# Kernel tuning notes

Hardware: AMD Instinct MI355X
Metric: run time of the kernel (lower is better)

Reference implementation:

```python
import jax, jax.numpy as jnp
import numpy as np

H = 128          # hidden_dim
L = 3            # num_layers
EPS = 1e-5       # BatchNorm eps


def setup_inputs() -> dict:
    key = jax.random.key(0)
    ks = jax.random.split(key, 12)
    B, N = 32, 8192
    s = 0.05
    x = jax.random.normal(ks[0], (B, N, 2), dtype=jnp.float32)
    mask = jnp.ones((B, N), dtype=jnp.float32)
    # parameters, stored as [in, out]
    emb_w = jax.random.normal(ks[1], (2, H), jnp.float32) * s
    emb_b = jnp.zeros((H,), jnp.float32)
    lin_w = jax.random.normal(ks[2], (L, H, H), jnp.float32) * s
    lin_b = jnp.zeros((L, H), jnp.float32)
    nb_w = jax.random.normal(ks[3], (L, H, H), jnp.float32) * s
    nb_b = jnp.zeros((L, H), jnp.float32)
    bn_g = jnp.ones((L, H), jnp.float32)
    bn_b = jnp.zeros((L, H), jnp.float32)
    out1_w = jax.random.normal(ks[4], (H, H // 2), jnp.float32) * s
    out1_b = jnp.zeros((H // 2,), jnp.float32)
    out2_w = jax.random.normal(ks[5], (H // 2, 2), jnp.float32) * s
    out2_b = jnp.zeros((2,), jnp.float32)
    return dict(x=x, mask=mask, emb_w=emb_w, emb_b=emb_b,
                lin_w=lin_w, lin_b=lin_b, nb_w=nb_w, nb_b=nb_b,
                bn_g=bn_g, bn_b=bn_b, out1_w=out1_w, out1_b=out1_b,
                out2_w=out2_w, out2_b=out2_b)


def reference(x, mask, emb_w, emb_b, lin_w, lin_b, nb_w, nb_b,
              bn_g, bn_b, out1_w, out1_b, out2_w, out2_b):
    m = mask[..., None]                     # [B, N, 1]
    h = x @ emb_w + emb_b                   # [B, N, H]
    for i in range(L):
        # graph conv: self transform + ring-neighbor (roll) transform
        nsum = jnp.roll(h, 1, axis=1) + jnp.roll(h, -1, axis=1)
        h_new = (h @ lin_w[i] + lin_b[i] + nsum @ nb_w[i] + nb_b[i]) * m
        # BatchNorm1d (training-mode batch stats over batch*nodes per channel)
        mean = jnp.mean(h_new, axis=(0, 1))
        var = jnp.mean(jnp.square(h_new - mean), axis=(0, 1))  # biased var
        h_new = (h_new - mean) * jax.lax.rsqrt(var + EPS) * bn_g[i] + bn_b[i]
        h_new = jax.nn.relu(h_new)          # dropout treated as identity (eval)
        h = h + h_new                       # residual
    out = jax.nn.relu(h @ out1_w + out1_b) @ out2_w + out2_b  # [B, N, 2]
    return out * m
```

## Files before the change

### kernel.cpp

```cpp
#include <hip/hip_runtime.h>
#include <cstddef>

#define H      128
#define NBATCH 32
#define NN     8192
#define RTOT   (NBATCH*NN)
#define NLAYER 3
#define BNEPS  1e-5f
#define NSLOT  16
#define CNPB   128
#define NTILEC (RTOT/CNPB)
#define HNPB   64
#define HS_STRIDE 136

typedef _Float16 f16;
typedef __attribute__((ext_vector_type(8))) _Float16 half8;
typedef __attribute__((ext_vector_type(4))) float f32x4;

__device__ __forceinline__ void unpackh8(uint4 pk, float* d) {
    const f16* hp = (const f16*)&pk;
    #pragma unroll
    for (int i = 0; i < 8; ++i) d[i] = (float)hp[i];
}
__device__ __forceinline__ uint4 packh8(const float* s) {
    uint4 pk;
    f16* hp = (f16*)&pk;
    #pragma unroll
    for (int i = 0; i < 8; ++i) hp[i] = (f16)s[i];
    return pk;
}

__device__ __forceinline__ void load_bfrags(
    const f16* __restrict__ Wt, half8 bW[2][4], int colbase, int l15, int quad)
{
    #pragma unroll
    for (int nt = 0; nt < 2; ++nt) {
        int nrow = colbase + nt * 16 + l15;
        #pragma unroll
        for (int ks = 0; ks < 4; ++ks)
            bW[nt][ks] = *((const half8*)(Wt + nrow * 128 + ks * 32 + quad * 8));
    }
}

__device__ __forceinline__ void conv_mfma8(
    const f16* __restrict__ hs, const half8 bWl[2][4], const half8 bWn[2][4],
    f32x4 acc[8][2], int l15, int quad)
{
    #pragma unroll
    for (int mt = 0; mt < 8; ++mt) {
        acc[mt][0] = (f32x4){0.f, 0.f, 0.f, 0.f};
        acc[mt][1] = (f32x4){0.f, 0.f, 0.f, 0.f};
    }
    #pragma unroll
    for (int ks = 0; ks < 4; ++ks) {
        #pragma unroll
        for (int mt = 0; mt < 8; ++mt) {
            int row = mt * 16 + l15;
            const f16* base = hs + row * HS_STRIDE + ks * 32 + quad * 8;
            half8 hm = *((const half8*)(base + HS_STRIDE));
            half8 hd = *((const half8*)(base));
            half8 hu = *((const half8*)(base + 2 * HS_STRIDE));
            half8 an = hd + hu;
            acc[mt][0] = __builtin_amdgcn_mfma_f32_16x16x32_f16(hm, bWl[0][ks], acc[mt][0], 0, 0, 0);
            acc[mt][1] = __builtin_amdgcn_mfma_f32_16x16x32_f16(hm, bWl[1][ks], acc[mt][1], 0, 0, 0);
            acc[mt][0] = __builtin_amdgcn_mfma_f32_16x16x32_f16(an, bWn[0][ks], acc[mt][0], 0, 0, 0);
            acc[mt][1] = __builtin_amdgcn_mfma_f32_16x16x32_f16(an, bWn[1][ks], acc[mt][1], 0, 0, 0);
        }
    }
}

__global__ __launch_bounds__(256) void k_prep(
    const float* __restrict__ lin_w, const float* __restrict__ nb_w,
    f16* __restrict__ Wlt, f16* __restrict__ Wnt)
{
    int id = blockIdx.x * 256 + threadIdx.x;
    int mat = id / 49152;
    int r   = id - mat * 49152;
    int l   = r >> 14;
    int r2  = r & 16383;
    int k   = r2 >> 7;
    int n   = r2 & 127;
    const float* src = mat ? nb_w : lin_w;
    f16*         dst = mat ? Wnt  : Wlt;
    dst[l * 16384 + n * 128 + k] = (f16)src[l * 16384 + k * 128 + n];
}

__device__ __forceinline__ void conv_epilogue_c(
    f32x4 acc[8][2], const float bsum[2], const float* __restrict__ msk,
    f16* __restrict__ hnb, float* __restrict__ gstats,
    int tile, int wave, int quad, int lane, int slot)
{
    uint2* out2 = (uint2*)hnb;
    float s[2] = {0.f, 0.f}, ss[2] = {0.f, 0.f};
    #pragma unroll
    for (int nt = 0; nt < 2; ++nt) {
        #pragma unroll
        for (int mt = 0; mt < 8; ++mt) {
            f16 v4[4];
            #pragma unroll
            for (int reg = 0; reg < 4; ++reg) {
                int lrow = mt * 16 + quad * 4 + reg;
                float v = (acc[mt][nt][reg] + bsum[nt]) * msk[lrow];
                v4[reg] = (f16)v;
                s[nt] += v; ss[nt] += v * v;
            }
            size_t chunk = ((size_t)tile * 4 + wave) * 16 + mt * 2 + nt;
            out2[chunk * 64 + lane] = *((const uint2*)v4);
        }
    }
    #pragma unroll
    for (int nt = 0; nt < 2; ++nt) {
        s[nt]  += __shfl_xor(s[nt], 16);  s[nt]  += __shfl_xor(s[nt], 32);
        ss[nt] += __shfl_xor(ss[nt], 16); ss[nt] += __shfl_xor(ss[nt], 32);
    }
    if (lane < 16) {
        int colbase = wave * 32;
        #pragma unroll
        for (int nt = 0; nt < 2; ++nt) {
            int col = colbase + nt * 16 + lane;
            atomicAdd(&gstats[slot * 2 * H + col],     s[nt]);
            atomicAdd(&gstats[slot * 2 * H + H + col], ss[nt]);
        }
    }
}

__device__ __forceinline__ void conv_epilogue_rm(
    f32x4 acc[8][2], const float bsum[2], const float* __restrict__ msk,
    f16* __restrict__ tr, f16* __restrict__ hnb, float* __restrict__ gstats,
    int r0, int colbase, int l15, int quad, int lane, int t, int slot)
{
    float s[2] = {0.f, 0.f}, ss[2] = {0.f, 0.f};
    #pragma unroll
    for (int nt = 0; nt < 2; ++nt) {
        int col = colbase + nt * 16 + l15;
        #pragma unroll
        for (int mt = 0; mt < 8; ++mt)
            #pragma unroll
            for (int reg = 0; reg < 4; ++reg) {
                int lrow = mt * 16 + quad * 4 + reg;
                float v = (acc[mt][nt][reg] + bsum[nt]) * msk[lrow];
                tr[lrow * HS_STRIDE + col] = (f16)v;
                s[nt] += v; ss[nt] += v * v;
            }
    }
    #pragma unroll
    for (int nt = 0; nt < 2; ++nt) {
        s[nt]  += __shfl_xor(s[nt], 16);  s[nt]  += __shfl_xor(s[nt], 32);
        ss[nt] += __shfl_xor(ss[nt], 16); ss[nt] += __shfl_xor(ss[nt], 32);
    }
    if (lane < 16)
        #pragma unroll
        for (int nt = 0; nt < 2; ++nt) {
            int col = colbase + nt * 16 + lane;
            atomicAdd(&gstats[slot * 2 * H + col],     s[nt]);
            atomicAdd(&gstats[slot * 2 * H + H + col], ss[nt]);
        }
    __syncthreads();
    for (int i = t; i < CNPB * 16; i += 256) {
        int row = i >> 4, g = i & 15;
        *((uint4*)(hnb + (size_t)(r0 + row) * H + g * 8)) =
            *((const uint4*)(tr + row * HS_STRIDE + g * 8));
    }
}

__global__ __launch_bounds__(256) void k_conv0f(
    const float* __restrict__ x, const float* __restrict__ ew,
    const float* __restrict__ eb,
    const f16* __restrict__ Wlt, const f16* __restrict__ Wnt,
    const float* __restrict__ bl, const float* __restrict__ bnb,
    const float* __restrict__ mask,
    f16* __restrict__ hnb, float* __restrict__ gstats)
{
    __shared__ __align__(16) f16 hs[(CNPB + 2) * HS_STRIDE];
    __shared__ float ews[3 * H], msk[CNPB];
    const int t = threadIdx.x, lane = t & 63;
    const int l15 = lane & 15, quad = lane >> 4;
    const int wave = t >> 6;
    const int colbase = wave * 32;
    const int r0 = blockIdx.x * CNPB;
    const int batch = r0 >> 13, n0 = r0 & (NN - 1);

    half8 bWl[2][4], bWn[2][4];
    load_bfrags(Wlt, bWl, colbase, l15, quad);
    load_bfrags(Wnt, bWn, colbase, l15, quad);
    float bsum[2];
    #pragma unroll
    for (int nt = 0; nt < 2; ++nt) {
        int col = colbase + nt * 16 + l15;
        bsum[nt] = bl[col] + bnb[col];
    }
    for (int c = t; c < H; c += 256) {
        ews[c] = ew[c]; ews[H + c] = ew[H + c]; ews[2 * H + c] = eb[c];
    }
    if (t < CNPB) msk[t] = mask[r0 + t];
    __syncthreads();

    for (int i = t; i < (CNPB + 2) * 16; i += 256) {
        int row = i >> 4, g = i & 15;
        int n = (n0 + row - 1 + NN) & (NN - 1);
        const float* xp = x + 2 * ((size_t)batch * NN + n);
        float x0 = xp[0], x1 = xp[1];
        f16 o[8];
        #pragma unroll
        for (int e = 0; e < 8; ++e) {
            int c = g * 8 + e;
            o[e] = (f16)fmaf(x1, ews[H + c], fmaf(x0, ews[c], ews[2 * H + c]));
        }
        *((uint4*)(hs + row * HS_STRIDE + g * 8)) = *((const uint4*)o);
    }
    __syncthreads();

    f32x4 acc[8][2];
    conv_mfma8(hs, bWl, bWn, acc, l15, quad);
    conv_epilogue_c(acc, bsum, msk, hnb, gstats,
                    blockIdx.x, wave, quad, lane, blockIdx.x & (NSLOT - 1));
}

__global__ __launch_bounds__(256) void k_conv0f_rm(
    const float* __restrict__ x, const float* __restrict__ ew,
    const float* __restrict__ eb,
    const f16* __restrict__ Wlt, const f16* __restrict__ Wnt,
    const float* __restrict__ bl, const float* __restrict__ bnb,
    const float* __restrict__ mask,
    f16* __restrict__ hnb, float* __restrict__ gstats)
{
    __shared__ __align__(16) f16 hs[(CNPB + 2) * HS_STRIDE];
    __shared__ float ews[3 * H], msk[CNPB];
    const int t = threadIdx.x, lane = t & 63;
    const int l15 = lane & 15, quad = lane >> 4;
    const int wave = t >> 6;
    const int colbase = wave * 32;
    const int r0 = blockIdx.x * CNPB;
    const int batch = r0 >> 13, n0 = r0 & (NN - 1);

    half8 bWl[2][4], bWn[2][4];
    load_bfrags(Wlt, bWl, colbase, l15, quad);
    load_bfrags(Wnt, bWn, colbase, l15, quad);
    float bsum[2];
    #pragma unroll
    for (int nt = 0; nt < 2; ++nt) {
        int col = colbase + nt * 16 + l15;
        bsum[nt] = bl[col] + bnb[col];
    }
    for (int c = t; c < H; c += 256) {
        ews[c] = ew[c]; ews[H + c] = ew[H + c]; ews[2 * H + c] = eb[c];
    }
    if (t < CNPB) msk[t] = mask[r0 + t];
    __syncthreads();

    for (int i = t; i < (CNPB + 2) * 16; i += 256) {
        int row = i >> 4, g = i & 15;
        int n = (n0 + row - 1 + NN) & (NN - 1);
        const float* xp = x + 2 * ((size_t)batch * NN + n);
        float x0 = xp[0], x1 = xp[1];
        f16 o[8];
        #pragma unroll
        for (int e = 0; e < 8; ++e) {
            int c = g * 8 + e;
            o[e] = (f16)fmaf(x1, ews[H + c], fmaf(x0, ews[c], ews[2 * H + c]));
        }
        *((uint4*)(hs + row * HS_STRIDE + g * 8)) = *((const uint4*)o);
    }
    __syncthreads();

    f32x4 acc[8][2];
    conv_mfma8(hs, bWl, bWn, acc, l15, quad);
    __syncthreads();
    conv_epilogue_rm(acc, bsum, msk, hs, hnb, gstats,
                     r0, colbase, l15, quad, lane, t, blockIdx.x & (NSLOT - 1));
}

__global__ __launch_bounds__(256) void k_conv(
    const f16* __restrict__ hb,
    const f16* __restrict__ Wlt, const f16* __restrict__ Wnt,
    const float* __restrict__ bl, const float* __restrict__ bnb,
    const float* __restrict__ mask,
    f16* __restrict__ hnb, float* __restrict__ gstats)
{
    __shared__ __align__(16) f16 hs[(CNPB + 2) * HS_STRIDE];
    __shared__ float msk[CNPB];
    const int t = threadIdx.x, lane = t & 63;
    const int l15 = lane & 15, quad = lane >> 4;
    const int wave = t >> 6;
    const int colbase = wave * 32;
    const int r0 = blockIdx.x * CNPB;
    const int batch = r0 >> 13, n0 = r0 & (NN - 1);

    half8 bWl[2][4], bWn[2][4];
    load_bfrags(Wlt, bWl, colbase, l15, quad);
    load_bfrags(Wnt, bWn, colbase, l15, quad);
    float bsum[2];
    #pragma unroll
    for (int nt = 0; nt < 2; ++nt) {
        int col = colbase + nt * 16 + l15;
        bsum[nt] = bl[col] + bnb[col];
    }
    if (t < CNPB) msk[t] = mask[r0 + t];

    for (int i = t; i < (CNPB + 2) * 16; i += 256) {
        int row = i >> 4, g = i & 15;
        int n = (n0 + row - 1 + NN) & (NN - 1);
        *((uint4*)(hs + row * HS_STRIDE + g * 8)) =
            *((const uint4*)(hb + ((size_t)(batch * NN + n)) * H + g * 8));
    }
    __syncthreads();

    f32x4 acc[8][2];
    conv_mfma8(hs, bWl, bWn, acc, l15, quad);
    conv_epilogue_c(acc, bsum, msk, hnb, gstats,
                    blockIdx.x, wave, quad, lane, blockIdx.x & (NSLOT - 1));
}

__global__ __launch_bounds__(256) void k_cn1(
    const float* __restrict__ x, const float* __restrict__ ew,
    const float* __restrict__ eb, const f16* __restrict__ hnA,
    const float* __restrict__ scl0,
    const f16* __restrict__ Wlt, const f16* __restrict__ Wnt,
    const float* __restrict__ bl, const float* __restrict__ bnb,
    const float* __restrict__ mask,
    f16* __restrict__ HB, f16* __restrict__ hnB, float* __restrict__ gst1)
{
    __shared__ __align__(16) f16 hs[(CNPB + 2) * HS_STRIDE];
    __shared__ float ews[3 * H], sclA[2 * H], msk[CNPB];
    const int t = threadIdx.x, lane = t & 63;
    const int l15 = lane & 15, quad = lane >> 4;
    const int wave = t >> 6;
    const int colbase = wave * 32;
    const int r0 = blockIdx.x * CNPB;
    const int batch = r0 >> 13, n0 = r0 & (NN - 1);

    half8 bWl[2][4], bWn[2][4];
    load_bfrags(Wlt, bWl, colbase, l15, quad);
    load_bfrags(Wnt, bWn, colbase, l15, quad);
    float bsum[2];
    #pragma unroll
    for (int nt = 0; nt < 2; ++nt) {
        int col = colbase + nt * 16 + l15;
        bsum[nt] = bl[col] + bnb[col];
    }
    for (int c = t; c < H; c += 256) {
        ews[c] = ew[c]; ews[H + c] = ew[H + c]; ews[2 * H + c] = eb[c];
        sclA[c] = scl0[c]; sclA[H + c] = scl0[H + c];
    }
    if (t < CNPB) msk[t] = mask[r0 + t];
    __syncthreads();

    for (int i = t; i < (CNPB + 2) * 16; i += 256) {
        int row = i >> 4, g = i & 15;
        int n = (n0 + row - 1 + NN) & (NN - 1);
        size_t base = (size_t)batch * NN + n;
        const float* xp = x + 2 * base;
        float x0 = xp[0], x1 = xp[1];
        uint4 pa = *((const uint4*)(hnA + base * H + g * 8));
        float va[8];
        unpackh8(pa, va);
        f16 o[8];
        #pragma unroll
        for (int e = 0; e < 8; ++e) {
            int c = g * 8 + e;
            float h0 = fmaf(x1, ews[H + c], fmaf(x0, ews[c], ews[2 * H + c]));
            o[e] = (f16)(h0 + fmaxf(fmaf(va[e], sclA[c], sclA[H + c]), 0.f));
        }
        *((uint4*)(hs + row * HS_STRIDE + g * 8)) = *((const uint4*)o);
    }
    __syncthreads();

    f32x4 acc[8][2];
    conv_mfma8(hs, bWl, bWn, acc, l15, quad);

    for (int i = t; i < CNPB * 16; i += 256) {
        int row = i >> 4, g = i & 15;
        *((uint4*)(HB + (size_t)(r0 + row) * H + g * 8)) =
            *((const uint4*)(hs + (row + 1) * HS_STRIDE + g * 8));
    }
    __syncthreads();

    conv_epilogue_rm(acc, bsum, msk, hs, hnB, gst1,
                     r0, colbase, l15, quad, lane, t, blockIdx.x & (NSLOT - 1));
}

__global__ __launch_bounds__(256) void k_cn2(
    const f16* __restrict__ HB, const f16* __restrict__ hnB,
    const float* __restrict__ scl1,
    const f16* __restrict__ Wlt, const f16* __restrict__ Wnt,
    const float* __restrict__ bl, const float* __restrict__ bnb,
    const float* __restrict__ mask,
    f16* __restrict__ hnA, float* __restrict__ gst2)
{
    __shared__ __align__(16) f16 hs[(CNPB + 2) * HS_STRIDE];
    __shared__ float sclA[2 * H], msk[CNPB];
    const int t = threadIdx.x, lane = t & 63;
    const int l15 = lane & 15, quad = lane >> 4;
    const int wave = t >> 6;
    const int colbase = wave * 32;
    const int r0 = blockIdx.x * CNPB;
    const int batch = r0 >> 13, n0 = r0 & (NN - 1);

    half8 bWl[2][4], bWn[2][4];
    load_bfrags(Wlt, bWl, colbase, l15, quad);
    load_bfrags(Wnt, bWn, colbase, l15, quad);
    float bsum[2];
    #pragma unroll
    for (int nt = 0; nt < 2; ++nt) {
        int col = colbase + nt * 16 + l15;
        bsum[nt] = bl[col] + bnb[col];
    }
    for (int c = t; c < H; c += 256) {
        sclA[c] = scl1[c]; sclA[H + c] = scl1[H + c];
    }
    if (t < CNPB) msk[t] = mask[r0 + t];
    __syncthreads();

    for (int i = t; i < (CNPB + 2) * 16; i += 256) {
        int row = i >> 4, g = i & 15;
        int n = (n0 + row - 1 + NN) & (NN - 1);
        size_t off = ((size_t)batch * NN + n) * H + g * 8;
        uint4 ph = *((const uint4*)(HB + off));
        uint4 pn = *((const uint4*)(hnB + off));
        float vh[8], vn[8];
        unpackh8(ph, vh);
        unpackh8(pn, vn);
        f16 o[8];
        #pragma unroll
        for (int e = 0; e < 8; ++e) {
            int c = g * 8 + e;
            o[e] = (f16)(vh[e] + fmaxf(fmaf(vn[e], sclA[c], sclA[H + c]), 0.f));
        }
        *((uint4*)(hs + row * HS_STRIDE + g * 8)) = *((const uint4*)o);
    }
    __syncthreads();

    f32x4 acc[8][2];
    conv_mfma8(hs, bWl, bWn, acc, l15, quad);
    __syncthreads();

    conv_epilogue_rm(acc, bsum, msk, hs, hnA, gst2,
                     r0, colbase, l15, quad, lane, t, blockIdx.x & (NSLOT - 1));
}

__global__ void k_fin(const float* __restrict__ gstats,
                      const float* __restrict__ g, const float* __restrict__ b,
                      float* __restrict__ o)
{
    int c = threadIdx.x;
    float s = 0.f, ss = 0.f;
    for (int i = 0; i < NSLOT; ++i) {
        s  += gstats[i * 2 * H + c];
        ss += gstats[i * 2 * H + H + c];
    }
    const float invR = 1.f / (float)RTOT;
    float mean = s * invR;
    float var  = ss * invR - mean * mean;
    float inv  = rsqrtf(var + BNEPS);
    float sc   = g[c] * inv;
    o[c] = sc;
    o[H + c] = fmaf(-mean, sc, b[c]);
}

__device__ __forceinline__ void norm_ingest(
    const f16* __restrict__ hnb, int blk, int t,
    const float* __restrict__ scl_s, const float* __restrict__ sft_s,
    f16* __restrict__ g)
{
    const uint4* src = (const uint4*)hnb + (size_t)blk * 2048;
    for (int i = t; i < 2048; i += 256) {
        uint4 pk = src[i];
        int chunk = i >> 5;
        int L     = (i & 31) * 2;
        int ntv   = chunk & 1;
        int mtv   = (chunk >> 1) & 7;
        int wv    = chunk >> 4;
        int c0    = wv * 32 + ntv * 16 + (L & 15);
        int row0  = mtv * 16 + (L >> 4) * 4;
        float vv[8];
        unpackh8(pk, vv);
        #pragma unroll
        for (int e = 0; e < 8; ++e) {
            int cc = c0 + (e >> 2);
            int rr = row0 + (e & 3);
            float q = fmaxf(fmaf(vv[e], scl_s[cc], sft_s[cc]), 0.f);
            g[rr * HS_STRIDE + cc] = (f16)q;
        }
    }
}

__device__ __forceinline__ void bn_finalize(
    const float* __restrict__ gstats, const float* __restrict__ bn_g,
    const float* __restrict__ bn_b, int t, float* scl_s, float* sft_s)
{
    if (t < H) {
        float s = 0.f, ss = 0.f;
        #pragma unroll
        for (int i = 0; i < NSLOT; ++i) {
            s  += gstats[i * 2 * H + t];
            ss += gstats[i * 2 * H + H + t];
        }
        const float invR = 1.f / (float)RTOT;
        float mean = s * invR;
        float var  = ss * invR - mean * mean;
        float inv  = rsqrtf(var + BNEPS);
        float sc   = bn_g[t] * inv;
        scl_s[t] = sc;
        sft_s[t] = fmaf(-mean, sc, bn_b[t]);
    }
}

__global__ __launch_bounds__(256) void k_norm0(
    const float* __restrict__ x, const float* __restrict__ ew,
    const float* __restrict__ eb, const f16* __restrict__ hnb,
    const float* __restrict__ gstats, const float* __restrict__ bn_g,
    const float* __restrict__ bn_b, f16* __restrict__ hb)
{
    __shared__ __align__(16) f16 g[CNPB * HS_STRIDE];
    __shared__ float scl_s[H], sft_s[H], ews[3 * H];
    const int t = threadIdx.x;
    const int blk = blockIdx.x;
    const size_t r0 = (size_t)blk * CNPB;

    bn_finalize(gstats, bn_g, bn_b, t, scl_s, sft_s);
    if (t < H) { ews[t] = ew[t]; ews[H + t] = ew[H + t]; ews[2 * H + t] = eb[t]; }
    __syncthreads();

    norm_ingest(hnb, blk, t, scl_s, sft_s, g);
    __syncthreads();

    for (int i = t; i < 2048; i += 256) {
        int row = i >> 4, gg = i & 15;
        size_t grow = r0 + row;
        float x0 = x[2 * grow], x1 = x[2 * grow + 1];
        uint4 pg = *((const uint4*)(g + row * HS_STRIDE + gg * 8));
        float vg[8], vh[8];
        unpackh8(pg, vg);
        #pragma unroll
        for (int e = 0; e < 8; ++e) {
            int c = gg * 8 + e;
            float h0 = fmaf(x1, ews[H + c], fmaf(x0, ews[c], ews[2 * H + c]));
            vh[e] = h0 + vg[e];
        }
        *((uint4*)(hb + grow * H + gg * 8)) = packh8(vh);
    }
}

__global__ __launch_bounds__(256) void k_norm(
    const f16* __restrict__ hnb, const float* __restrict__ gstats,
    const float* __restrict__ bn_g, const float* __restrict__ bn_b,
    f16* __restrict__ hb)
{
    __shared__ __align__(16) f16 g[CNPB * HS_STRIDE];
    __shared__ float scl_s[H], sft_s[H];
    const int t = threadIdx.x;
    const int blk = blockIdx.x;
    const size_t r0 = (size_t)blk * CNPB;

    bn_finalize(gstats, bn_g, bn_b, t, scl_s, sft_s);
    __syncthreads();

    norm_ingest(hnb, blk, t, scl_s, sft_s, g);
    __syncthreads();

    for (int i = t; i < 2048; i += 256) {
        int row = i >> 4, gg = i & 15;
        size_t grow = r0 + row;
        uint4 ph = *((const uint4*)(hb + grow * H + gg * 8));
        uint4 pg = *((const uint4*)(g + row * HS_STRIDE + gg * 8));
        float vh[8], vg[8];
        unpackh8(ph, vh);
        unpackh8(pg, vg);
        #pragma unroll
        for (int e = 0; e < 8; ++e) vh[e] += vg[e];
        *((uint4*)(hb + grow * H + gg * 8)) = packh8(vh);
    }
}

__global__ __launch_bounds__(256) void k_head(
    const f16* __restrict__ hb, const float* __restrict__ W1,
    const float* __restrict__ b1, const float* __restrict__ W2,
    const float* __restrict__ b2, const float* __restrict__ mask,
    float* __restrict__ out)
{
    __shared__ f16 hs [64 * HS_STRIDE];
    __shared__ f16 w1t[64 * HS_STRIDE];
    const int t    = threadIdx.x;
    const int wave = t >> 6;
    const int lane = t & 63;
    const int l15  = lane & 15;
    const int quad = lane >> 4;
    const int r0   = blockIdx.x * HNPB;

    for (int i = t; i < 64 * 16; i += 256) {
        int row = i >> 4, g = i & 15;
        *((uint4*)(hs + row * HS_STRIDE + g * 8)) =
            *((const uint4*)(hb + (size_t)(r0 + row) * H + g * 8));
    }
    for (int i = t; i < H * 64; i += 256) {
        int k = i >> 6, n = i & 63;
        w1t[n * HS_STRIDE + k] = (f16)W1[i];
    }
    __syncthreads();

    f32x4 acc[4];
    #pragma unroll
    for (int nt = 0; nt < 4; ++nt) acc[nt] = (f32x4){0.f, 0.f, 0.f, 0.f};
    #pragma unroll
    for (int ks = 0; ks < 4; ++ks) {
        half8 a = *((const half8*)(hs + (wave * 16 + l15) * HS_STRIDE + ks * 32 + quad * 8));
        #pragma unroll
        for (int nt = 0; nt < 4; ++nt) {
            half8 b = *((const half8*)(w1t + (nt * 16 + l15) * HS_STRIDE + ks * 32 + quad * 8));
            acc[nt] = __builtin_amdgcn_mfma_f32_16x16x32_f16(a, b, acc[nt], 0, 0, 0);
        }
    }

    float p0[4] = {0,0,0,0}, p1[4] = {0,0,0,0};
    #pragma unroll
    for (int nt = 0; nt < 4; ++nt) {
        int col = nt * 16 + l15;
        float bb = b1[col];
        float wa = W2[2 * col], wb = W2[2 * col + 1];
        #pragma unroll
        for (int reg = 0; reg < 4; ++reg) {
            float v = fmaxf(acc[nt][reg] + bb, 0.f);
            p0[reg] = fmaf(v, wa, p0[reg]);
            p1[reg] = fmaf(v, wb, p1[reg]);
        }
    }
    #pragma unroll
    for (int reg = 0; reg < 4; ++reg) {
        p0[reg] += __shfl_xor(p0[reg], 1); p0[reg] += __shfl_xor(p0[reg], 2);
        p0[reg] += __shfl_xor(p0[reg], 4); p0[reg] += __shfl_xor(p0[reg], 8);
        p1[reg] += __shfl_xor(p1[reg], 1); p1[reg] += __shfl_xor(p1[reg], 2);
        p1[reg] += __shfl_xor(p1[reg], 4); p1[reg] += __shfl_xor(p1[reg], 8);
    }
    if (l15 == 0) {
        #pragma unroll
        for (int reg = 0; reg < 4; ++reg) {
            int gr = r0 + wave * 16 + quad * 4 + reg;
            float m = mask[gr];
            float2 o;
            o.x = (p0[reg] + b2[0]) * m;
            o.y = (p1[reg] + b2[1]) * m;
            *((float2*)(out + 2 * gr)) = o;
        }
    }
}

__global__ __launch_bounds__(256) void k_head_f(
    const f16* __restrict__ HB, const f16* __restrict__ hn1,
    const f16* __restrict__ hn2, const float* __restrict__ sclb,
    const float* __restrict__ W1, const float* __restrict__ b1,
    const float* __restrict__ W2, const float* __restrict__ b2,
    const float* __restrict__ mask, float* __restrict__ out)
{
    __shared__ f16 hs [64 * HS_STRIDE];
    __shared__ f16 w1t[64 * HS_STRIDE];
    __shared__ float sclA[4 * H];
    const int t    = threadIdx.x;
    const int wave = t >> 6;
    const int lane = t & 63;
    const int l15  = lane & 15;
    const int quad = lane >> 4;
    const int r0   = blockIdx.x * HNPB;

    for (int i = t; i < 4 * H; i += 256) sclA[i] = sclb[i];
    for (int i = t; i < H * 64; i += 256) {
        int k = i >> 6, n = i & 63;
        w1t[n * HS_STRIDE + k] = (f16)W1[i];
    }
    __syncthreads();

    for (int i = t; i < 64 * 16; i += 256) {
        int row = i >> 4, g = i & 15;
        size_t off = (size_t)(r0 + row) * H + g * 8;
        uint4 ph = *((const uint4*)(HB + off));
        uint4 p1v = *((const uint4*)(hn1 + off));
        uint4 p2v = *((const uint4*)(hn2 + off));
        float vh[8], v1[8], v2[8];
        unpackh8(ph, vh);
        unpackh8(p1v, v1);
        unpackh8(p2v, v2);
        f16 o[8];
        #pragma unroll
        for (int e = 0; e < 8; ++e) {
            int c = g * 8 + e;
            float h2 = vh[e] + fmaxf(fmaf(v1[e], sclA[c],         sclA[H + c]),     0.f);
            o[e] = (f16)(h2 + fmaxf(fmaf(v2[e], sclA[2 * H + c], sclA[3 * H + c]), 0.f));
        }
        *((uint4*)(hs + row * HS_STRIDE + g * 8)) = *((const uint4*)o);
    }
    __syncthreads();

    f32x4 acc[4];
    #pragma unroll
    for (int nt = 0; nt < 4; ++nt) acc[nt] = (f32x4){0.f, 0.f, 0.f, 0.f};
    #pragma unroll
    for (int ks = 0; ks < 4; ++ks) {
        half8 a = *((const half8*)(hs + (wave * 16 + l15) * HS_STRIDE + ks * 32 + quad * 8));
        #pragma unroll
        for (int nt = 0; nt < 4; ++nt) {
            half8 b = *((const half8*)(w1t + (nt * 16 + l15) * HS_STRIDE + ks * 32 + quad * 8));
            acc[nt] = __builtin_amdgcn_mfma_f32_16x16x32_f16(a, b, acc[nt], 0, 0, 0);
        }
    }

    float p0[4] = {0,0,0,0}, p1a[4] = {0,0,0,0};
    #pragma unroll
    for (int nt = 0; nt < 4; ++nt) {
        int col = nt * 16 + l15;
        float bb = b1[col];
        float wa = W2[2 * col], wb = W2[2 * col + 1];
        #pragma unroll
        for (int reg = 0; reg < 4; ++reg) {
            float v = fmaxf(acc[nt][reg] + bb, 0.f);
            p0[reg]  = fmaf(v, wa, p0[reg]);
            p1a[reg] = fmaf(v, wb, p1a[reg]);
        }
    }
    #pragma unroll
    for (int reg = 0; reg < 4; ++reg) {
        p0[reg]  += __shfl_xor(p0[reg], 1);  p0[reg]  += __shfl_xor(p0[reg], 2);
        p0[reg]  += __shfl_xor(p0[reg], 4);  p0[reg]  += __shfl_xor(p0[reg], 8);
        p1a[reg] += __shfl_xor(p1a[reg], 1); p1a[reg] += __shfl_xor(p1a[reg], 2);
        p1a[reg] += __shfl_xor(p1a[reg], 4); p1a[reg] += __shfl_xor(p1a[reg], 8);
    }
    if (l15 == 0) {
        #pragma unroll
        for (int reg = 0; reg < 4; ++reg) {
            int gr = r0 + wave * 16 + quad * 4 + reg;
            float m = mask[gr];
            float2 o;
            o.x = (p0[reg]  + b2[0]) * m;
            o.y = (p1a[reg] + b2[1]) * m;
            *((float2*)(out + 2 * gr)) = o;
        }
    }
}

extern "C" void kernel_launch(void* const* d_in, const int* in_sizes, int n_in,
                              void* d_out, int out_size, void* d_ws, size_t ws_size,
                              hipStream_t stream)
{
    const float* x     = (const float*)d_in[0];
    const float* mask  = (const float*)d_in[1];
    const float* emb_w = (const float*)d_in[2];
    const float* emb_b = (const float*)d_in[3];
    const float* lin_w = (const float*)d_in[4];
    const float* lin_b = (const float*)d_in[5];
    const float* nb_w  = (const float*)d_in[6];
    const float* nb_b  = (const float*)d_in[7];
    const float* bn_g  = (const float*)d_in[8];
    const float* bn_b  = (const float*)d_in[9];
    const float* o1w   = (const float*)d_in[10];
    const float* o1b   = (const float*)d_in[11];
    const float* o2w   = (const float*)d_in[12];
    const float* o2b   = (const float*)d_in[13];
    float* out = (float*)d_out;

    const size_t BUF = (size_t)RTOT * H * 2;
    char* ws = (char*)d_ws;

    float* gst = (float*)d_out;
    f16* Wlt = (f16*)((float*)d_out + 65536);
    f16* Wnt = Wlt + NLAYER * H * H;

    hipMemsetAsync(gst, 0, NLAYER * NSLOT * 2 * H * sizeof(float), stream);
    k_prep<<<384, 256, 0, stream>>>(lin_w, nb_w, Wlt, Wnt);

    if (ws_size >= 3 * BUF + 65536) {
        f16* HB  = (f16*)ws;
        f16* hnA = (f16*)(ws + BUF);
        f16* hnB = (f16*)(ws + 2 * BUF);
        float* sclbuf = (float*)(ws + 3 * BUF);

        k_conv0f_rm<<<NTILEC, 256, 0, stream>>>(
            x, emb_w, emb_b, Wlt, Wnt, lin_b, nb_b, mask, hnA, gst);
        k_fin<<<1, H, 0, stream>>>(gst, bn_g, bn_b, sclbuf);
        k_cn1<<<NTILEC, 256, 0, stream>>>(
            x, emb_w, emb_b, hnA, sclbuf, Wlt + H * H, Wnt + H * H,
            lin_b + H, nb_b + H, mask, HB, hnB, gst + NSLOT * 2 * H);
        k_fin<<<1, H, 0, stream>>>(gst + NSLOT * 2 * H, bn_g + H, bn_b + H,
                                   sclbuf + 2 * H);
        k_cn2<<<NTILEC, 256, 0, stream>>>(
            HB, hnB, sclbuf + 2 * H, Wlt + 2 * H * H, Wnt + 2 * H * H,
            lin_b + 2 * H, nb_b + 2 * H, mask, hnA, gst + 2 * NSLOT * 2 * H);
        k_fin<<<1, H, 0, stream>>>(gst + 2 * NSLOT * 2 * H, bn_g + 2 * H,
                                   bn_b + 2 * H, sclbuf + 4 * H);
        k_head_f<<<RTOT / HNPB, 256, 0, stream>>>(
            HB, hnB, hnA, sclbuf + 2 * H, o1w, o1b, o2w, o2b, mask, out);
    } else {
        f16* hb  = (f16*)ws;
        f16* hnb = (f16*)(ws + BUF);

        k_conv0f<<<NTILEC, 256, 0, stream>>>(
            x, emb_w, emb_b, Wlt, Wnt, lin_b, nb_b, mask, hnb, gst);
        k_norm0<<<NTILEC, 256, 0, stream>>>(
            x, emb_w, emb_b, hnb, gst, bn_g, bn_b, hb);
        for (int i = 1; i < NLAYER; ++i) {
            k_conv<<<NTILEC, 256, 0, stream>>>(
                hb, Wlt + i * H * H, Wnt + i * H * H,
                lin_b + i * H, nb_b + i * H, mask,
                hnb, gst + i * NSLOT * 2 * H);
            k_norm<<<NTILEC, 256, 0, stream>>>(
                hnb, gst + i * NSLOT * 2 * H, bn_g + i * H, bn_b + i * H, hb);
        }
        k_head<<<RTOT / HNPB, 256, 0, stream>>>(hb, o1w, o1b, o2w, o2b, mask, out);
    }
}
```

Measured before the change: 323.7 us.

## Fold BatchNorm finalize into consumer kernels and write residual during staging

Removes the three single-block k_fin launches by having each consumer kernel (k_cn1, k_cn2, k_head_f) reduce the per-slot BN statistics itself into shared memory at block start. Moves the stats buffer into the workspace and writes the layer-1 residual HB directly while staging tiles, which drops a separate copy loop after the MFMA. It also adds a 3-blocks-per-CU occupancy hint to k_cn1. The cost is that every block now redundantly reads 16 slots of stats and does the rsqrt work, and the head kernel does this for two layers.

```diff
diff --git a/kernel.cpp b/kernel.cpp
--- a/kernel.cpp
+++ b/kernel.cpp
@@ -85,6 +85,27 @@
     dst[l * 16384 + n * 128 + k] = (f16)src[l * 16384 + k * 128 + n];
 }
 
+__device__ __forceinline__ void bn_finalize(
+    const float* __restrict__ gstats, const float* __restrict__ bn_g,
+    const float* __restrict__ bn_b, int t, float* scl_s, float* sft_s)
+{
+    if (t < H) {
+        float s = 0.f, ss = 0.f;
+        #pragma unroll
+        for (int i = 0; i < NSLOT; ++i) {
+            s  += gstats[i * 2 * H + t];
+            ss += gstats[i * 2 * H + H + t];
+        }
+        const float invR = 1.f / (float)RTOT;
+        float mean = s * invR;
+        float var  = ss * invR - mean * mean;
+        float inv  = rsqrtf(var + BNEPS);
+        float sc   = bn_g[t] * inv;
+        scl_s[t] = sc;
+        sft_s[t] = fmaf(-mean, sc, bn_b[t]);
+    }
+}
+
 __device__ __forceinline__ void conv_epilogue_c(
     f32x4 acc[8][2], const float bsum[2], const float* __restrict__ msk,
     f16* __restrict__ hnb, float* __restrict__ gstats,
@@ -311,17 +332,18 @@
                     blockIdx.x, wave, quad, lane, blockIdx.x & (NSLOT - 1));
 }
 
-__global__ __launch_bounds__(256) void k_cn1(
+__global__ __launch_bounds__(256, 3) void k_cn1(
     const float* __restrict__ x, const float* __restrict__ ew,
     const float* __restrict__ eb, const f16* __restrict__ hnA,
-    const float* __restrict__ scl0,
+    const float* __restrict__ gst0, const float* __restrict__ bn_g,
+    const float* __restrict__ bn_b,
     const f16* __restrict__ Wlt, const f16* __restrict__ Wnt,
     const float* __restrict__ bl, const float* __restrict__ bnb,
     const float* __restrict__ mask,
     f16* __restrict__ HB, f16* __restrict__ hnB, float* __restrict__ gst1)
 {
     __shared__ __align__(16) f16 hs[(CNPB + 2) * HS_STRIDE];
-    __shared__ float ews[3 * H], sclA[2 * H], msk[CNPB];
+    __shared__ float ews[3 * H], sclA[H], sftA[H], msk[CNPB];
     const int t = threadIdx.x, lane = t & 63;
     const int l15 = lane & 15, quad = lane >> 4;
     const int wave = t >> 6;
@@ -338,9 +360,9 @@
         int col = colbase + nt * 16 + l15;
         bsum[nt] = bl[col] + bnb[col];
     }
+    bn_finalize(gst0, bn_g, bn_b, t, sclA, sftA);
     for (int c = t; c < H; c += 256) {
         ews[c] = ew[c]; ews[H + c] = ew[H + c]; ews[2 * H + c] = eb[c];
-        sclA[c] = scl0[c]; sclA[H + c] = scl0[H + c];
     }
     if (t < CNPB) msk[t] = mask[r0 + t];
     __syncthreads();
@@ -359,20 +381,16 @@
         for (int e = 0; e < 8; ++e) {
             int c = g * 8 + e;
             float h0 = fmaf(x1, ews[H + c], fmaf(x0, ews[c], ews[2 * H + c]));
-            o[e] = (f16)(h0 + fmaxf(fmaf(va[e], sclA[c], sclA[H + c]), 0.f));
+            o[e] = (f16)(h0 + fmaxf(fmaf(va[e], sclA[c], sftA[c]), 0.f));
         }
         *((uint4*)(hs + row * HS_STRIDE + g * 8)) = *((const uint4*)o);
+        if (row >= 1 && row <= CNPB)
+            *((uint4*)(HB + base * H + g * 8)) = *((const uint4*)o);
     }
     __syncthreads();
 
     f32x4 acc[8][2];
     conv_mfma8(hs, bWl, bWn, acc, l15, quad);
-
-    for (int i = t; i < CNPB * 16; i += 256) {
-        int row = i >> 4, g = i & 15;
-        *((uint4*)(HB + (size_t)(r0 + row) * H + g * 8)) =
-            *((const uint4*)(hs + (row + 1) * HS_STRIDE + g * 8));
-    }
     __syncthreads();
 
     conv_epilogue_rm(acc, bsum, msk, hs, hnB, gst1,
@@ -381,14 +399,15 @@
 
 __global__ __launch_bounds__(256) void k_cn2(
     const f16* __restrict__ HB, const f16* __restrict__ hnB,
-    const float* __restrict__ scl1,
+    const float* __restrict__ gst1, const float* __restrict__ bn_g,
+    const float* __restrict__ bn_b,
     const f16* __restrict__ Wlt, const f16* __restrict__ Wnt,
     const float* __restrict__ bl, const float* __restrict__ bnb,
     const float* __restrict__ mask,
     f16* __restrict__ hnA, float* __restrict__ gst2)
 {
     __shared__ __align__(16) f16 hs[(CNPB + 2) * HS_STRIDE];
-    __shared__ float sclA[2 * H], msk[CNPB];
+    __shared__ float sclA[H], sftA[H], msk[CNPB];
     const int t = threadIdx.x, lane = t & 63;
     const int l15 = lane & 15, quad = lane >> 4;
     const int wave = t >> 6;
@@ -405,9 +424,7 @@
         int col = colbase + nt * 16 + l15;
         bsum[nt] = bl[col] + bnb[col];
     }
-    for (int c = t; c < H; c += 256) {
-        sclA[c] = scl1[c]; sclA[H + c] = scl1[H + c];
-    }
+    bn_finalize(gst1, bn_g, bn_b, t, sclA, sftA);
     if (t < CNPB) msk[t] = mask[r0 + t];
     __syncthreads();
 
@@ -424,7 +441,7 @@
         #pragma unroll
         for (int e = 0; e < 8; ++e) {
             int c = g * 8 + e;
-            o[e] = (f16)(vh[e] + fmaxf(fmaf(vn[e], sclA[c], sclA[H + c]), 0.f));
+            o[e] = (f16)(vh[e] + fmaxf(fmaf(vn[e], sclA[c], sftA[c]), 0.f));
         }
         *((uint4*)(hs + row * HS_STRIDE + g * 8)) = *((const uint4*)o);
     }
@@ -436,25 +453,6 @@
 
     conv_epilogue_rm(acc, bsum, msk, hs, hnA, gst2,
                      r0, colbase, l15, quad, lane, t, blockIdx.x & (NSLOT - 1));
-}
-
-__global__ void k_fin(const float* __restrict__ gstats,
-                      const float* __restrict__ g, const float* __restrict__ b,
-                      float* __restrict__ o)
-{
-    int c = threadIdx.x;
-    float s = 0.f, ss = 0.f;
-    for (int i = 0; i < NSLOT; ++i) {
-        s  += gstats[i * 2 * H + c];
-        ss += gstats[i * 2 * H + H + c];
-    }
-    const float invR = 1.f / (float)RTOT;
-    float mean = s * invR;
-    float var  = ss * invR - mean * mean;
-    float inv  = rsqrtf(var + BNEPS);
-    float sc   = g[c] * inv;
-    o[c] = sc;
-    o[H + c] = fmaf(-mean, sc, b[c]);
 }
 
 __device__ __forceinline__ void norm_ingest(
@@ -484,27 +482,6 @@
     }
 }
 
-__device__ __forceinline__ void bn_finalize(
-    const float* __restrict__ gstats, const float* __restrict__ bn_g,
-    const float* __restrict__ bn_b, int t, float* scl_s, float* sft_s)
-{
-    if (t < H) {
-        float s = 0.f, ss = 0.f;
-        #pragma unroll
-        for (int i = 0; i < NSLOT; ++i) {
-            s  += gstats[i * 2 * H + t];
-            ss += gstats[i * 2 * H + H + t];
-        }
-        const float invR = 1.f / (float)RTOT;
-        float mean = s * invR;
-        float var  = ss * invR - mean * mean;
-        float inv  = rsqrtf(var + BNEPS);
-        float sc   = bn_g[t] * inv;
-        scl_s[t] = sc;
-        sft_s[t] = fmaf(-mean, sc, bn_b[t]);
-    }
-}
-
 __global__ __launch_bounds__(256) void k_norm0(
     const float* __restrict__ x, const float* __restrict__ ew,
     const float* __restrict__ eb, const f16* __restrict__ hnb,
@@ -646,14 +623,16 @@
 
 __global__ __launch_bounds__(256) void k_head_f(
     const f16* __restrict__ HB, const f16* __restrict__ hn1,
-    const f16* __restrict__ hn2, const float* __restrict__ sclb,
+    const f16* __restrict__ hn2,
+    const float* __restrict__ gst1, const float* __restrict__ gst2,
+    const float* __restrict__ bn_g, const float* __restrict__ bn_b,
     const float* __restrict__ W1, const float* __restrict__ b1,
     const float* __restrict__ W2, const float* __restrict__ b2,
     const float* __restrict__ mask, float* __restrict__ out)
 {
     __shared__ f16 hs [64 * HS_STRIDE];
     __shared__ f16 w1t[64 * HS_STRIDE];
-    __shared__ float sclA[4 * H];
+    __shared__ float scl1[H], sft1[H], scl2[H], sft2[H];
     const int t    = threadIdx.x;
     const int wave = t >> 6;
     const int lane = t & 63;
@@ -661,7 +640,8 @@
     const int quad = lane >> 4;
     const int r0   = blockIdx.x * HNPB;
 
-    for (int i = t; i < 4 * H; i += 256) sclA[i] = sclb[i];
+    bn_finalize(gst1, bn_g,     bn_b,     t, scl1, sft1);
+    bn_finalize(gst2, bn_g + H, bn_b + H, t, scl2, sft2);
     for (int i = t; i < H * 64; i += 256) {
         int k = i >> 6, n = i & 63;
         w1t[n * HS_STRIDE + k] = (f16)W1[i];
@@ -682,8 +662,8 @@
         #pragma unroll
         for (int e = 0; e < 8; ++e) {
             int c = g * 8 + e;
-            float h2 = vh[e] + fmaxf(fmaf(v1[e], sclA[c],         sclA[H + c]),     0.f);
-            o[e] = (f16)(h2 + fmaxf(fmaf(v2[e], sclA[2 * H + c], sclA[3 * H + c]), 0.f));
+            float h2 = vh[e] + fmaxf(fmaf(v1[e], scl1[c], sft1[c]), 0.f);
+            o[e] = (f16)(h2 + fmaxf(fmaf(v2[e], scl2[c], sft2[c]), 0.f));
         }
         *((uint4*)(hs + row * HS_STRIDE + g * 8)) = *((const uint4*)o);
     }
@@ -756,39 +736,39 @@
     float* out = (float*)d_out;
 
     const size_t BUF = (size_t)RTOT * H * 2;
+    const size_t GSTB = NLAYER * NSLOT * 2 * H * sizeof(float);
     char* ws = (char*)d_ws;
 
-    float* gst = (float*)d_out;
     f16* Wlt = (f16*)((float*)d_out + 65536);
     f16* Wnt = Wlt + NLAYER * H * H;
-
-    hipMemsetAsync(gst, 0, NLAYER * NSLOT * 2 * H * sizeof(float), stream);
     k_prep<<<384, 256, 0, stream>>>(lin_w, nb_w, Wlt, Wnt);
 
     if (ws_size >= 3 * BUF + 65536) {
         f16* HB  = (f16*)ws;
         f16* hnA = (f16*)(ws + BUF);
         f16* hnB = (f16*)(ws + 2 * BUF);
-        float* sclbuf = (float*)(ws + 3 * BUF);
+        float* gstw = (float*)(ws + 3 * BUF);
+
+        hipMemsetAsync(gstw, 0, GSTB, stream);
 
         k_conv0f_rm<<<NTILEC, 256, 0, stream>>>(
-            x, emb_w, emb_b, Wlt, Wnt, lin_b, nb_b, mask, hnA, gst);
-        k_fin<<<1, H, 0, stream>>>(gst, bn_g, bn_b, sclbuf);
+            x, emb_w, emb_b, Wlt, Wnt, lin_b, nb_b, mask, hnA, gstw);
         k_cn1<<<NTILEC, 256, 0, stream>>>(
-            x, emb_w, emb_b, hnA, sclbuf, Wlt + H * H, Wnt + H * H,
-            lin_b + H, nb_b + H, mask, HB, hnB, gst + NSLOT * 2 * H);
-        k_fin<<<1, H, 0, stream>>>(gst + NSLOT * 2 * H, bn_g + H, bn_b + H,
-                                   sclbuf + 2 * H);
+            x, emb_w, emb_b, hnA, gstw, bn_g, bn_b, Wlt + H * H, Wnt + H * H,
+            lin_b + H, nb_b + H, mask, HB, hnB, gstw + NSLOT * 2 * H);
         k_cn2<<<NTILEC, 256, 0, stream>>>(
-            HB, hnB, sclbuf + 2 * H, Wlt + 2 * H * H, Wnt + 2 * H * H,
-            lin_b + 2 * H, nb_b + 2 * H, mask, hnA, gst + 2 * NSLOT * 2 * H);
-        k_fin<<<1, H, 0, stream>>>(gst + 2 * NSLOT * 2 * H, bn_g + 2 * H,
-                                   bn_b + 2 * H, sclbuf + 4 * H);
+            HB, hnB, gstw + NSLOT * 2 * H, bn_g + H, bn_b + H,
+            Wlt + 2 * H * H, Wnt + 2 * H * H,
+            lin_b + 2 * H, nb_b + 2 * H, mask, hnA, gstw + 2 * NSLOT * 2 * H);
         k_head_f<<<RTOT / HNPB, 256, 0, stream>>>(
-            HB, hnB, hnA, sclbuf + 2 * H, o1w, o1b, o2w, o2b, mask, out);
+            HB, hnB, hnA, gstw + NSLOT * 2 * H, gstw + 2 * NSLOT * 2 * H,
+            bn_g + H, bn_b + H, o1w, o1b, o2w, o2b, mask, out);
     } else {
+        float* gst = (float*)d_out;
         f16* hb  = (f16*)ws;
         f16* hnb = (f16*)(ws + BUF);
+
+        hipMemsetAsync(gst, 0, GSTB, stream);
 
         k_conv0f<<<NTILEC, 256, 0, stream>>>(
             x, emb_w, emb_b, Wlt, Wnt, lin_b, nb_b, mask, hnb, gst);
```

Measured after the change: 294.4 us. -9.0%, faster.
